# Kernel optimization log

Hardware: AMD Instinct MI355X
Metric: run time of the kernel (lower is better)

The kernel has to match this reference:

```python
import jax, jax.numpy as jnp
import numpy as np

E = 1024   # embed_dim
H = 16     # num_heads
D = E // H # head_dim = 64
B = 2
S = 2048

def setup_inputs() -> dict:
    key = jax.random.key(0)
    ks = jax.random.split(key, 11)
    std = 0.02
    return {
        "query": jax.random.normal(ks[0], (B, S, E), jnp.float32),
        "key":   jax.random.normal(ks[1], (B, S, E), jnp.float32),
        "value": jax.random.normal(ks[2], (B, S, E), jnp.float32),
        "Wq": std * jax.random.normal(ks[3], (E, E), jnp.float32),
        "bq": jnp.zeros((E,), jnp.float32),
        "Wk": std * jax.random.normal(ks[4], (D, E), jnp.float32),
        "bk": jnp.zeros((D,), jnp.float32),
        "Wv": std * jax.random.normal(ks[5], (D, E), jnp.float32),
        "bv": jnp.zeros((D,), jnp.float32),
        "Wo": std * jax.random.normal(ks[6], (E, E), jnp.float32),
        "bo": jnp.zeros((E,), jnp.float32),
    }

def reference(query, key, value, Wq, bq, Wk, bk, Wv, bv, Wo, bo):
    b, t, _ = query.shape
    scaling = D ** -0.5
    q = query @ Wq.T + bq                      # [B, T, E]
    k = key @ Wk.T + bk                        # [B, S, D] (single shared KV head)
    v = value @ Wv.T + bv                      # [B, S, D]
    q = q.reshape(b, t, H, D).transpose(0, 2, 1, 3) * scaling  # [B, H, T, D]
    # MQA: broadcast shared k/v across heads inside einsum (no materialized expand)
    attn_weights = jnp.einsum("bhtd,bsd->bhts", q, k)          # [B, H, T, S]
    attn_probs = jax.nn.softmax(attn_weights, axis=-1)
    attn_output = jnp.einsum("bhts,bsd->bhtd", attn_probs, v)  # [B, H, T, D]
    attn_output = attn_output.transpose(0, 2, 1, 3).reshape(b, t, E)
    return attn_output @ Wo.T + bo
```

## Files before the change

kernel.cpp:

```cpp
#include <hip/hip_runtime.h>

#define E_DIM  1024
#define H_HEADS 16
#define D_HEAD  64
#define B_BATCH 2
#define S_SEQ  2048
#define M_ROWS (B_BATCH * S_SEQ)

typedef unsigned short u16;
typedef unsigned int   u32;
typedef __attribute__((ext_vector_type(8))) short bf16x8;
typedef __attribute__((ext_vector_type(4))) short bf16x4;
typedef __attribute__((ext_vector_type(4))) float f32x4;

#define MFMA32(a, b, c) __builtin_amdgcn_mfma_f32_16x16x32_bf16(a, b, c, 0, 0, 0)

#if __has_builtin(__builtin_amdgcn_mfma_f32_16x16x16bf16_1k)
#define HAVE_MFMA16 1
#define MFMA16(a, b, c) __builtin_amdgcn_mfma_f32_16x16x16bf16_1k(a, b, c, 0, 0, 0)
#else
#define HAVE_MFMA16 0
#endif

__device__ __forceinline__ u16 f2bf(float f) {
    union { float f; u32 i; } x; x.f = f;
    u32 r = x.i + 0x7fffu + ((x.i >> 16) & 1u);
    return (u16)(r >> 16);
}

#if __has_builtin(__builtin_amdgcn_cvt_pk_bf16_f32)
typedef __attribute__((ext_vector_type(2))) __bf16 bfp2;
__device__ __forceinline__ u32 pk2(float a, float b) {
    bfp2 t = __builtin_amdgcn_cvt_pk_bf16_f32(a, b);
    union { bfp2 v; u32 u; } c; c.v = t; return c.u;
}
#else
__device__ __forceinline__ u32 pk2(float a, float b) {
    return (u32)f2bf(a) | ((u32)f2bf(b) << 16);
}
#endif

__device__ __forceinline__ bf16x8 cvt8(const float4& a, const float4& b) {
    union { u32 u[4]; bf16x8 v; } t;
    t.u[0] = pk2(a.x, a.y); t.u[1] = pk2(a.z, a.w);
    t.u[2] = pk2(b.x, b.y); t.u[3] = pk2(b.z, b.w);
    return t.v;
}
__device__ __forceinline__ bf16x4 pack4(const f32x4& v) {
    union { u32 u[2]; bf16x4 w; } t;
    t.u[0] = pk2(v[0], v[1]); t.u[1] = pk2(v[2], v[3]);
    return t.w;
}

__device__ __forceinline__ void gl_lds16(const u16* g, u16* l) {
    __builtin_amdgcn_global_load_lds(
        (const __attribute__((address_space(1))) u32*)g,
        (__attribute__((address_space(3))) u32*)l, 16, 0, 0);
}

__global__ __launch_bounds__(256) void prep_kernel(
    const float* __restrict__ query, const float* __restrict__ Wq,
    const float* __restrict__ Wo,
    u16* __restrict__ qc, u16* __restrict__ wq_bf, u16* __restrict__ wo_bf,
    const float* __restrict__ key, const float* __restrict__ value,
    const float* __restrict__ Wk, const float* __restrict__ Wv,
    const float* __restrict__ bk, const float* __restrict__ bv,
    u16* __restrict__ Kout, u16* __restrict__ VTout, int M, int K)
{
    __shared__ u16 Asm[64 * 32];
    __shared__ u16 Bsm[64 * 32];

    const int bid = blockIdx.x;
    const int tid = threadIdx.x;

    if (bid >= 128) {
        const int cbid = bid - 128;
        const float* src; u16* dst; size_t base;
        if (cbid < 2048)      { src = query; dst = qc;    base = (size_t)cbid * 2048; }
        else if (cbid < 2560) { src = Wq;    dst = wq_bf; base = (size_t)(cbid - 2048) * 2048; }
        else                  { src = Wo;    dst = wo_bf; base = (size_t)(cbid - 2560) * 2048; }
        const size_t i = base + (size_t)tid * 8;
        float4 a = ((const float4*)(src + i))[0];
        float4 b = ((const float4*)(src + i))[1];
        *(bf16x8*)(dst + i) = cvt8(a, b);
        return;
    }

    const bool vproj = (bid >= 64);
    const float* A    = vproj ? value : key;
    const float* W    = vproj ? Wv : Wk;
    const float* bias = vproj ? bv : bk;

    const int w  = tid >> 6;
    const int ln = tid & 63;
    const int n  = ln & 15;
    const int qd = ln >> 4;
    const int wm = (w & 1) * 32;
    const int wn = (w >> 1) * 32;
    const int m0 = (bid & 63) * 64;

    const int srow = tid >> 2;
    const int scol = (tid & 3) * 8;

    f32x4 acc[2][2];
#pragma unroll
    for (int mt = 0; mt < 2; mt++)
#pragma unroll
        for (int nt = 0; nt < 2; nt++) acc[mt][nt] = (f32x4){0.f, 0.f, 0.f, 0.f};

    for (int k0 = 0; k0 < K; k0 += 32) {
        __syncthreads();
        const float* pa = A + (size_t)(m0 + srow) * K + k0 + scol;
        const float* pw = W + (size_t)srow * K + k0 + scol;
        float4 a0 = ((const float4*)pa)[0], a1 = ((const float4*)pa)[1];
        float4 w0 = ((const float4*)pw)[0], w1 = ((const float4*)pw)[1];
        *(bf16x8*)&Asm[srow * 32 + scol] = cvt8(a0, a1);
        *(bf16x8*)&Bsm[srow * 32 + scol] = cvt8(w0, w1);
        __syncthreads();

        bf16x8 af[2], bfr[2];
#pragma unroll
        for (int t = 0; t < 2; t++) {
            af[t]  = *(const bf16x8*)&Asm[(wm + t * 16 + n) * 32 + qd * 8];
            bfr[t] = *(const bf16x8*)&Bsm[(wn + t * 16 + n) * 32 + qd * 8];
        }
#pragma unroll
        for (int mt = 0; mt < 2; mt++)
#pragma unroll
            for (int nt = 0; nt < 2; nt++)
                acc[mt][nt] = MFMA32(af[mt], bfr[nt], acc[mt][nt]);
    }

    if (!vproj) {
#pragma unroll
        for (int mt = 0; mt < 2; mt++)
#pragma unroll
            for (int r = 0; r < 4; r++) {
                const int row = m0 + wm + mt * 16 + qd * 4 + r;
#pragma unroll
                for (int nt = 0; nt < 2; nt++) {
                    const int col = wn + nt * 16 + n;
                    Kout[(size_t)row * 64 + col] = f2bf(acc[mt][nt][r] + bias[col]);
                }
            }
    } else {
#pragma unroll
        for (int mt = 0; mt < 2; mt++)
#pragma unroll
            for (int nt = 0; nt < 2; nt++) {
                const int col = wn + nt * 16 + n;
                const int row0 = m0 + wm + mt * 16 + qd * 4;
                float b4 = bias[col];
                ushort4 pk;
                pk.x = f2bf(acc[mt][nt][0] + b4);
                pk.y = f2bf(acc[mt][nt][1] + b4);
                pk.z = f2bf(acc[mt][nt][2] + b4);
                pk.w = f2bf(acc[mt][nt][3] + b4);
                *(ushort4*)&VTout[(size_t)col * M + row0] = pk;
            }
    }
}

template<bool OUT_BF16>
__global__ __launch_bounds__(256, 2) void gemm_bf16_kernel(
    const u16* __restrict__ A, const u16* __restrict__ W,
    const float* __restrict__ bias, void* __restrict__ Cv,
    int M, int N, int K, float scale)
{
    __shared__ u16 Asm[2][2][128 * 32];
    __shared__ u16 Bsm[2][2][64 * 32];

    const int tid = threadIdx.x;
    const int w  = tid >> 6;
    const int ln = tid & 63;
    const int n  = ln & 15;
    const int qd = ln >> 4;
    const int ns = (n & 3) ^ (n >> 2);
    const int wm = (w & 1) * 64;
    const int wn = (w >> 1) * 32;

    const int m0 = blockIdx.y * 128;
    const int n0 = blockIdx.x * 64;

    const int srow = tid >> 2;
    const int sblk = tid & 3;
    const int sc   = ((sblk ^ (srow & 3) ^ ((srow >> 2) & 3)) * 8);

    f32x4 acc[4][2];
#pragma unroll
    for (int mt = 0; mt < 4; mt++)
#pragma unroll
        for (int nt = 0; nt < 2; nt++) acc[mt][nt] = (f32x4){0.f, 0.f, 0.f, 0.f};

    auto stageA = [&](int p, int k0) {
#pragma unroll
        for (int kb = 0; kb < 2; kb++)
#pragma unroll
            for (int g = 0; g < 2; g++) {
                const int row = g * 64 + srow;
                gl_lds16(A + (size_t)(m0 + row) * K + k0 + kb * 32 + sc,
                         &Asm[p][kb][row * 32 + sblk * 8]);
            }
    };
    auto stageB = [&](int p, int k0) {
#pragma unroll
        for (int kb = 0; kb < 2; kb++)
            gl_lds16(W + (size_t)(n0 + srow) * K + k0 + kb * 32 + sc,
                     &Bsm[p][kb][srow * 32 + sblk * 8]);
    };
    auto compute = [&](int p) {
        bf16x8 af[4][2], bfr[2][2];
#pragma unroll
        for (int kb = 0; kb < 2; kb++) {
#pragma unroll
            for (int mt = 0; mt < 4; mt++) {
                const int r = wm + mt * 16 + n;
                af[mt][kb] = *(const bf16x8*)&Asm[p][kb][r * 32 + ((qd ^ ns) * 8)];
            }
#pragma unroll
            for (int nt = 0; nt < 2; nt++) {
                const int r = wn + nt * 16 + n;
                bfr[nt][kb] = *(const bf16x8*)&Bsm[p][kb][r * 32 + ((qd ^ ns) * 8)];
            }
        }
#pragma unroll
        for (int kb = 0; kb < 2; kb++)
#pragma unroll
            for (int mt = 0; mt < 4; mt++)
#pragma unroll
                for (int nt = 0; nt < 2; nt++)
                    acc[mt][nt] = MFMA32(af[mt][kb], bfr[nt][kb], acc[mt][nt]);
    };

    stageA(0, 0); stageB(0, 0);

    int p = 0;
    for (int k0 = 64; k0 < K; k0 += 64) {
        __syncthreads();
        stageA(p ^ 1, k0);
        stageB(p ^ 1, k0);
        compute(p);
        p ^= 1;
    }
    __syncthreads();
    compute(p);

    float bb[2];
#pragma unroll
    for (int nt = 0; nt < 2; nt++) bb[nt] = bias[n0 + wn + nt * 16 + n] * scale;

#pragma unroll
    for (int mt = 0; mt < 4; mt++)
#pragma unroll
        for (int r = 0; r < 4; r++) {
            const int row = m0 + wm + mt * 16 + qd * 4 + r;
#pragma unroll
            for (int nt = 0; nt < 2; nt++) {
                const int col = n0 + wn + nt * 16 + n;
                float v = acc[mt][nt][r] * scale + bb[nt];
                if (OUT_BF16) ((u16*)Cv)[(size_t)row * N + col] = f2bf(v);
                else        ((float*)Cv)[(size_t)row * N + col] = v;
            }
        }
}

__global__ __launch_bounds__(256, 2) void mqa_attn_mfma_kernel(
    const u16* Q, const u16* __restrict__ K,
    const u16* __restrict__ VT, u16* O)
{
    __shared__ u16 ksm[2][2][128 * 32];
    __shared__ u16 vsm[2][4][64 * 32];
#if !HAVE_MFMA16
    __shared__ u16 psm[4][32 * 128];
#endif

    const int tid = threadIdx.x;
    const int w   = tid >> 6;
    const int ln  = tid & 63;
    const int n   = ln & 15;
    const int qd  = ln >> 4;
    const int lr  = ln >> 2;
    const int blk = ln & 3;
    const int ns  = (n & 3) ^ (n >> 2);
    const int rs  = (lr & 3) ^ (lr >> 2);

    const int bid = blockIdx.x;
    const int qb = bid & 15;
    const int h  = (bid >> 4) & (H_HEADS - 1);
    const int b  = bid >> 8;
    const int q0 = qb * 128;

    const u16* kg = K  + (size_t)b * S_SEQ * 64;
    const u16* vg = VT + (size_t)b * S_SEQ;

    auto stageKV = [&](int p, int s0) {
#pragma unroll
        for (int kb = 0; kb < 2; kb++)
#pragma unroll
            for (int j = 0; j < 2; j++) {
                int row = w * 32 + j * 16 + lr;
                gl_lds16(kg + (size_t)(s0 + row) * 64 + kb * 32 + ((blk ^ rs) * 8),
                         &ksm[p][kb][row * 32 + blk * 8]);
            }
#pragma unroll
        for (int j = 0; j < 4; j++) {
            int d = j * 16 + lr;
            gl_lds16(vg + (size_t)d * M_ROWS + s0 + w * 32 + ((blk ^ rs) * 8),
                     &vsm[p][w][d * 32 + blk * 8]);
        }
    };

    {
        const u16* qg = Q + (size_t)(b * S_SEQ + q0) * E_DIM + h * 64;
#pragma unroll
        for (int kb = 0; kb < 2; kb++)
#pragma unroll
            for (int j = 0; j < 2; j++) {
                int row = w * 32 + j * 16 + lr;
                gl_lds16(qg + (size_t)row * E_DIM + kb * 32 + ((blk ^ rs) * 8),
                         &ksm[1][kb][row * 32 + blk * 8]);
            }
    }
    __syncthreads();

    bf16x8 qa[2][2];
#pragma unroll
    for (int mt = 0; mt < 2; mt++)
#pragma unroll
        for (int kb = 0; kb < 2; kb++) {
            int row = w * 32 + mt * 16 + n;
            qa[mt][kb] = *(const bf16x8*)&ksm[1][kb][row * 32 + ((qd ^ ns) * 8)];
        }

    stageKV(0, 0);

    f32x4 acc_o[2][4];
    float lsum[2] = {0.f, 0.f};
#pragma unroll
    for (int mt = 0; mt < 2; mt++)
#pragma unroll
        for (int ntd = 0; ntd < 4; ntd++) acc_o[mt][ntd] = (f32x4){0.f, 0.f, 0.f, 0.f};

    int p = 0;
    for (int s0 = 0; s0 < S_SEQ; s0 += 128) {
        __syncthreads();
        if (s0 + 128 < S_SEQ) stageKV(p ^ 1, s0 + 128);

        f32x4 sacc[2][8];
#pragma unroll
        for (int mt = 0; mt < 2; mt++)
#pragma unroll
            for (int nt = 0; nt < 8; nt++) sacc[mt][nt] = (f32x4){0.f, 0.f, 0.f, 0.f};
#pragma unroll
        for (int nt = 0; nt < 8; nt++) {
            int rowk = nt * 16 + n;
#pragma unroll
            for (int kb = 0; kb < 2; kb++) {
                bf16x8 kf = *(const bf16x8*)&ksm[p][kb][rowk * 32 + ((qd ^ ns) * 8)];
                sacc[0][nt] = MFMA32(kf, qa[0][kb], sacc[0][nt]);
                sacc[1][nt] = MFMA32(kf, qa[1][kb], sacc[1][nt]);
            }
        }

        bf16x4 pa[2][8];
#pragma unroll
        for (int mt = 0; mt < 2; mt++) {
            float ls = 0.f;
#pragma unroll
            for (int nt = 0; nt < 8; nt++) {
#pragma unroll
                for (int r = 0; r < 4; r++) {
                    float pv = exp2f(sacc[mt][nt][r]);
                    sacc[mt][nt][r] = pv;
                    ls += pv;
                }
                pa[mt][nt] = pack4(sacc[mt][nt]);
            }
            lsum[mt] += ls;
        }

#if HAVE_MFMA16
#pragma unroll
        for (int kk = 0; kk < 8; kk++) {
            int c = kk >> 1;
            int lblk = (kk & 1) * 2 + (qd >> 1);
#pragma unroll
            for (int ntd = 0; ntd < 4; ntd++) {
                int d = ntd * 16 + n;
                bf16x4 bv = *(const bf16x4*)
                    &vsm[p][c][d * 32 + ((lblk ^ ns) * 8) + (qd & 1) * 4];
                acc_o[0][ntd] = MFMA16(pa[0][kk], bv, acc_o[0][ntd]);
                acc_o[1][ntd] = MFMA16(pa[1][kk], bv, acc_o[1][ntd]);
            }
        }
#else
#pragma unroll
        for (int mt = 0; mt < 2; mt++)
#pragma unroll
            for (int nt = 0; nt < 8; nt++) {
                int t = mt * 16 + n;
                int lb = nt * 2 + (qd >> 1);
                union { bf16x4 v; uint2 u; } pw; pw.v = pa[mt][nt];
                *(uint2*)&psm[w][t * 128 + ((lb ^ n) * 8) + (qd & 1) * 4] = pw.u;
            }
        __syncthreads();
#pragma unroll
        for (int kb = 0; kb < 4; kb++) {
            bf16x8 paf[2];
#pragma unroll
            for (int mt = 0; mt < 2; mt++) {
                int t = mt * 16 + n;
                paf[mt] = *(const bf16x8*)&psm[w][t * 128 + (((kb * 4 + qd) ^ n) * 8)];
            }
#pragma unroll
            for (int ntd = 0; ntd < 4; ntd++) {
                int d = ntd * 16 + n;
                bf16x8 bv = *(const bf16x8*)&vsm[p][kb][d * 32 + ((qd ^ ns) * 8)];
                acc_o[0][ntd] = MFMA32(paf[0], bv, acc_o[0][ntd]);
                acc_o[1][ntd] = MFMA32(paf[1], bv, acc_o[1][ntd]);
            }
        }
#endif
        p ^= 1;
    }

#pragma unroll
    for (int mt = 0; mt < 2; mt++) {
        lsum[mt] += __shfl_xor(lsum[mt], 16);
        lsum[mt] += __shfl_xor(lsum[mt], 32);
    }
#pragma unroll
    for (int mt = 0; mt < 2; mt++)
#pragma unroll
        for (int r = 0; r < 4; r++) {
            float inv = 1.f / __shfl(lsum[mt], qd * 4 + r);
            int grow = b * S_SEQ + q0 + w * 32 + mt * 16 + qd * 4 + r;
#pragma unroll
            for (int ntd = 0; ntd < 4; ntd++) {
                int gcol = h * D_HEAD + ntd * 16 + n;
                O[(size_t)grow * E_DIM + gcol] = f2bf(acc_o[mt][ntd][r] * inv);
            }
        }
}

extern "C" void kernel_launch(void* const* d_in, const int* in_sizes, int n_in,
                              void* d_out, int out_size, void* d_ws, size_t ws_size,
                              hipStream_t stream) {
    const float* query = (const float*)d_in[0];
    const float* key   = (const float*)d_in[1];
    const float* value = (const float*)d_in[2];
    const float* Wq    = (const float*)d_in[3];
    const float* bq    = (const float*)d_in[4];
    const float* Wk    = (const float*)d_in[5];
    const float* bk    = (const float*)d_in[6];
    const float* Wv    = (const float*)d_in[7];
    const float* bv    = (const float*)d_in[8];
    const float* Wo    = (const float*)d_in[9];
    const float* bo    = (const float*)d_in[10];
    float* out = (float*)d_out;

    const int M = M_ROWS;

    u16* q_bf  = (u16*)d_ws;
    u16* k_bf  = q_bf + (size_t)M * E_DIM;
    u16* vt_bf = k_bf + (size_t)M * D_HEAD;
    u16* wq_bf = vt_bf + (size_t)M * D_HEAD;
    u16* wo_bf = wq_bf + (size_t)E_DIM * E_DIM;

    u16* qc_bf = (u16*)d_out;

    dim3 blk(256);
    const float scaling = 0.125f * 1.44269504088896f;

    prep_kernel<<<dim3(3200), blk, 0, stream>>>(
        query, Wq, Wo, qc_bf, wq_bf, wo_bf,
        key, value, Wk, Wv, bk, bv, k_bf, vt_bf, M, E_DIM);

    gemm_bf16_kernel<true><<<dim3(E_DIM / 64, M / 128), blk, 0, stream>>>(
        qc_bf, wq_bf, bq, q_bf, M, E_DIM, E_DIM, scaling);

    mqa_attn_mfma_kernel<<<dim3(B_BATCH * H_HEADS * (S_SEQ / 128)), blk, 0, stream>>>(
        q_bf, k_bf, vt_bf, q_bf);

    gemm_bf16_kernel<false><<<dim3(E_DIM / 64, M / 128), blk, 0, stream>>>(
        q_bf, wo_bf, bo, out, M, E_DIM, E_DIM, 1.0f);
}
```

Baseline: 248.6 us.

## Triple-buffer GEMM LDS staging and double-buffer K/V projection loads

The bf16 GEMM goes from a double-buffered to a triple-buffered LDS ring. Loads are issued two tiles ahead, and each step waits with an explicit partial vmcnt wait plus a raw barrier, so global-to-LDS copies overlap more compute. The K/V projection in the prep kernel now prefetches the next K-slice into registers and writes it to a second LDS buffer after the MFMAs, hiding global load latency. The cost is more LDS per block, which may reduce occupancy at 2 blocks/CU. The hand-counted vmcnt value is fragile if the number of loads per stage changes.

```diff
diff --git a/kernel.cpp b/kernel.cpp
--- a/kernel.cpp
+++ b/kernel.cpp
@@ -67,8 +67,8 @@
     const float* __restrict__ bk, const float* __restrict__ bv,
     u16* __restrict__ Kout, u16* __restrict__ VTout, int M, int K)
 {
-    __shared__ u16 Asm[64 * 32];
-    __shared__ u16 Bsm[64 * 32];
+    __shared__ u16 Asm[2][64 * 32];
+    __shared__ u16 Bsm[2][64 * 32];
 
     const int bid = blockIdx.x;
     const int tid = threadIdx.x;
@@ -108,27 +108,39 @@
 #pragma unroll
         for (int nt = 0; nt < 2; nt++) acc[mt][nt] = (f32x4){0.f, 0.f, 0.f, 0.f};
 
-    for (int k0 = 0; k0 < K; k0 += 32) {
-        __syncthreads();
+    float4 a0, a1, w0, w1;
+    auto loadT = [&](int k0) {
         const float* pa = A + (size_t)(m0 + srow) * K + k0 + scol;
         const float* pw = W + (size_t)srow * K + k0 + scol;
-        float4 a0 = ((const float4*)pa)[0], a1 = ((const float4*)pa)[1];
-        float4 w0 = ((const float4*)pw)[0], w1 = ((const float4*)pw)[1];
-        *(bf16x8*)&Asm[srow * 32 + scol] = cvt8(a0, a1);
-        *(bf16x8*)&Bsm[srow * 32 + scol] = cvt8(w0, w1);
+        a0 = ((const float4*)pa)[0]; a1 = ((const float4*)pa)[1];
+        w0 = ((const float4*)pw)[0]; w1 = ((const float4*)pw)[1];
+    };
+
+    const int nk = K / 32;
+    loadT(0);
+    *(bf16x8*)&Asm[0][srow * 32 + scol] = cvt8(a0, a1);
+    *(bf16x8*)&Bsm[0][srow * 32 + scol] = cvt8(w0, w1);
+
+    for (int t = 0; t < nk; ++t) {
+        if (t + 1 < nk) loadT((t + 1) * 32);
         __syncthreads();
 
         bf16x8 af[2], bfr[2];
 #pragma unroll
-        for (int t = 0; t < 2; t++) {
-            af[t]  = *(const bf16x8*)&Asm[(wm + t * 16 + n) * 32 + qd * 8];
-            bfr[t] = *(const bf16x8*)&Bsm[(wn + t * 16 + n) * 32 + qd * 8];
+        for (int t2 = 0; t2 < 2; t2++) {
+            af[t2]  = *(const bf16x8*)&Asm[t & 1][(wm + t2 * 16 + n) * 32 + qd * 8];
+            bfr[t2] = *(const bf16x8*)&Bsm[t & 1][(wn + t2 * 16 + n) * 32 + qd * 8];
         }
 #pragma unroll
         for (int mt = 0; mt < 2; mt++)
 #pragma unroll
             for (int nt = 0; nt < 2; nt++)
                 acc[mt][nt] = MFMA32(af[mt], bfr[nt], acc[mt][nt]);
+
+        if (t + 1 < nk) {
+            *(bf16x8*)&Asm[(t + 1) & 1][srow * 32 + scol] = cvt8(a0, a1);
+            *(bf16x8*)&Bsm[(t + 1) & 1][srow * 32 + scol] = cvt8(w0, w1);
+        }
     }
 
     if (!vproj) {
@@ -167,8 +179,8 @@
     const float* __restrict__ bias, void* __restrict__ Cv,
     int M, int N, int K, float scale)
 {
-    __shared__ u16 Asm[2][2][128 * 32];
-    __shared__ u16 Bsm[2][2][64 * 32];
+    __shared__ u16 Asm[3][2][128 * 32];
+    __shared__ u16 Bsm[3][2][64 * 32];
 
     const int tid = threadIdx.x;
     const int w  = tid >> 6;
@@ -192,7 +204,7 @@
 #pragma unroll
         for (int nt = 0; nt < 2; nt++) acc[mt][nt] = (f32x4){0.f, 0.f, 0.f, 0.f};
 
-    auto stageA = [&](int p, int k0) {
+    auto stage = [&](int p, int k0) {
 #pragma unroll
         for (int kb = 0; kb < 2; kb++)
 #pragma unroll
@@ -201,8 +213,6 @@
                 gl_lds16(A + (size_t)(m0 + row) * K + k0 + kb * 32 + sc,
                          &Asm[p][kb][row * 32 + sblk * 8]);
             }
-    };
-    auto stageB = [&](int p, int k0) {
 #pragma unroll
         for (int kb = 0; kb < 2; kb++)
             gl_lds16(W + (size_t)(n0 + srow) * K + k0 + kb * 32 + sc,
@@ -232,18 +242,29 @@
                     acc[mt][nt] = MFMA32(af[mt][kb], bfr[nt][kb], acc[mt][nt]);
     };
 
-    stageA(0, 0); stageB(0, 0);
-
-    int p = 0;
-    for (int k0 = 64; k0 < K; k0 += 64) {
-        __syncthreads();
-        stageA(p ^ 1, k0);
-        stageB(p ^ 1, k0);
-        compute(p);
-        p ^= 1;
-    }
-    __syncthreads();
-    compute(p);
+    const int nt_tiles = K / 64;
+    stage(0, 0);
+    stage(1, 64);
+
+    int pc = 0, ps = 2;
+    for (int t = 0; t + 2 < nt_tiles; ++t) {
+        asm volatile("s_waitcnt vmcnt(6)" ::: "memory");
+        __builtin_amdgcn_s_barrier();
+        __builtin_amdgcn_sched_barrier(0);
+        stage(ps, (t + 2) * 64);
+        compute(pc);
+        pc = (pc == 2) ? 0 : pc + 1;
+        ps = (ps == 2) ? 0 : ps + 1;
+    }
+    asm volatile("s_waitcnt vmcnt(6)" ::: "memory");
+    __builtin_amdgcn_s_barrier();
+    __builtin_amdgcn_sched_barrier(0);
+    compute(pc);
+    pc = (pc == 2) ? 0 : pc + 1;
+    asm volatile("s_waitcnt vmcnt(0)" ::: "memory");
+    __builtin_amdgcn_s_barrier();
+    __builtin_amdgcn_sched_barrier(0);
+    compute(pc);
 
     float bb[2];
 #pragma unroll
```

Measured after the change: 249.8 us. Within noise of the previous version (+0.5%).
